# Performance work log

Measured on AMD Instinct MI355X. Metric: run time of the kernel, lower is better.

## Reference

```python
import jax, jax.numpy as jnp
import numpy as np

N = 262144  # nodes
E = 262144  # edges (child -> parent)
X = 128     # x_size
H = 128     # h_size


def setup_inputs() -> dict:
    key = jax.random.key(0)
    ks = jax.random.split(key, 10)
    s = 1.0 / np.sqrt(H)
    return {
        "token_embeds": jax.random.normal(ks[0], (N, X), jnp.float32),
        "h": jax.random.normal(ks[1], (N, H), jnp.float32),
        "c": jax.random.normal(ks[2], (N, H), jnp.float32),
        "src": jax.random.randint(ks[3], (E,), 0, N),
        "dst": jax.random.randint(ks[4], (E,), 0, N),
        "W_iou": jax.random.normal(ks[5], (3 * H, X), jnp.float32) * s,
        "U_iou": jax.random.normal(ks[6], (3 * H, H), jnp.float32) * s,
        "b_iou": jnp.zeros((1, 3 * H), jnp.float32),
        "U_f_w": jax.random.normal(ks[7], (H, H), jnp.float32) * s,
        "U_f_b": jnp.zeros((H,), jnp.float32),
        "W_f_w": jax.random.normal(ks[8], (H, X), jnp.float32) * s,
        "b_f": jnp.zeros((1, H), jnp.float32),
    }


def reference(token_embeds, h, c, src, dst, W_iou, U_iou, b_iou, U_f_w, U_f_b, W_f_w, b_f):
    # message + reduce: gather children's h/c and sum into parent mailboxes
    h_sum = jax.ops.segment_sum(h[src], dst, num_segments=N)  # [N,H]
    c_sum = jax.ops.segment_sum(c[src], dst, num_segments=N)  # [N,H]
    # forget gate is per-node, so sum_k f*c_k == f * sum_k c_k
    f = jax.nn.sigmoid(token_embeds @ W_f_w.T + h @ U_f_w.T + U_f_b + b_f)  # [N,H]
    c_red = f * c_sum
    iou = token_embeds @ W_iou.T + h_sum @ U_iou.T + b_iou  # [N,3H]
    i, o, u = jnp.split(iou, 3, axis=1)
    c_new = jax.nn.sigmoid(i) * jnp.tanh(u) + c_red
    h_new = jax.nn.sigmoid(o) * jnp.tanh(c_new)
    return h_new, c_new
```

## Files before the change

kernel.cpp:

```cpp
#include <hip/hip_runtime.h>
#include <hip/hip_bf16.h>
#include <cstdint>

#define HH 128
#define XX 128

typedef __attribute__((ext_vector_type(8))) short short8;
typedef __attribute__((ext_vector_type(4))) short short4_;
typedef __attribute__((ext_vector_type(4))) float float4_;
typedef __attribute__((ext_vector_type(8))) _Float16 half8_;

__device__ __forceinline__ float sigmoidf_(float x) {
  return 1.f / (1.f + __expf(-x));
}
__device__ __forceinline__ float tanhf_(float x) {
  float e = __expf(-2.f * fabsf(x));
  float t = (1.f - e) / (1.f + e);
  return copysignf(t, x);
}

__global__ __launch_bounds__(256) void hist_kernel(const int* __restrict__ dst,
                                                   int* __restrict__ cnt, int E) {
  int e = blockIdx.x * 256 + threadIdx.x;
  if (e < E) atomicAdd(&cnt[dst[e]], 1);
}

__global__ __launch_bounds__(256) void scan_block_sum(const int* __restrict__ cnt,
                                                      int* __restrict__ bsum) {
  __shared__ int red[256];
  int b = blockIdx.x, t = threadIdx.x;
  int base = b * 1024 + t * 4;
  int s = cnt[base] + cnt[base + 1] + cnt[base + 2] + cnt[base + 3];
  red[t] = s;
  __syncthreads();
  for (int off = 128; off > 0; off >>= 1) {
    if (t < off) red[t] += red[t + off];
    __syncthreads();
  }
  if (t == 0) bsum[b] = red[0];
}

__global__ __launch_bounds__(256) void scan_top(const int* __restrict__ bsum,
                                                int* __restrict__ boff,
                                                int* __restrict__ row_ptr, int N,
                                                int E) {
  __shared__ int tmp[256];
  int t = threadIdx.x;
  int own = bsum[t];
  tmp[t] = own;
  __syncthreads();
  for (int off = 1; off < 256; off <<= 1) {
    int x = (t >= off) ? tmp[t - off] : 0;
    __syncthreads();
    tmp[t] += x;
    __syncthreads();
  }
  boff[t] = tmp[t] - own;
  if (t == 0) row_ptr[N] = E;
}

__global__ __launch_bounds__(256) void scan_fill(const int* __restrict__ cnt,
                                                 const int* __restrict__ boff,
                                                 int* __restrict__ row_ptr,
                                                 int* __restrict__ row_fill) {
  __shared__ int tsum[256];
  int b = blockIdx.x, t = threadIdx.x;
  int base = b * 1024 + t * 4;
  int v0 = cnt[base], v1 = cnt[base + 1], v2 = cnt[base + 2], v3 = cnt[base + 3];
  int s = v0 + v1 + v2 + v3;
  tsum[t] = s;
  __syncthreads();
  for (int off = 1; off < 256; off <<= 1) {
    int x = (t >= off) ? tsum[t - off] : 0;
    __syncthreads();
    tsum[t] += x;
    __syncthreads();
  }
  int excl = tsum[t] - s + boff[b];
  int p0 = excl, p1 = p0 + v0, p2 = p1 + v1, p3 = p2 + v2;
  row_ptr[base] = p0;
  row_ptr[base + 1] = p1;
  row_ptr[base + 2] = p2;
  row_ptr[base + 3] = p3;
  row_fill[base] = p0;
  row_fill[base + 1] = p1;
  row_fill[base + 2] = p2;
  row_fill[base + 3] = p3;
}

__global__ __launch_bounds__(256) void fill_kernel(const int* __restrict__ src,
                                                   const int* __restrict__ dst,
                                                   int* __restrict__ row_fill,
                                                   int* __restrict__ edge_src,
                                                   int E) {
  int e = blockIdx.x * 256 + threadIdx.x;
  if (e >= E) return;
  int pos = atomicAdd(&row_fill[dst[e]], 1);
  edge_src[pos] = src[e];
}

__global__ __launch_bounds__(256) void prep_kernel(
    const float* __restrict__ W_iou, const float* __restrict__ U_iou,
    const float* __restrict__ b_iou, const float* __restrict__ U_f_w,
    const float* __restrict__ U_f_b, const float* __restrict__ W_f_w,
    const float* __restrict__ b_f, unsigned short* __restrict__ Bh,
    float* __restrict__ bias) {
  int tid = blockIdx.x * 256 + threadIdx.x;
  int kg = tid & 3;
  int c16 = (tid >> 2) & 15;
  int ks = (tid >> 6) & 7;
  int w = (tid >> 9) & 7;
  int g = (tid >> 12) & 3;
  int col = w * 16 + c16;
  int kbase = ks * 32 + kg * 8;
#pragma unroll
  for (int j = 0; j < 8; ++j) {
    int k = kbase + j;
    float v;
    if (g < 3) {
      v = (k < 128) ? W_iou[(size_t)(g * 128 + col) * 128 + k]
                    : U_iou[(size_t)(g * 128 + col) * 128 + (k - 128)];
    } else {
      v = (k < 128) ? W_f_w[(size_t)col * 128 + k]
                    : U_f_w[(size_t)col * 128 + (k - 128)];
    }
    Bh[(size_t)tid * 8 + j] = __builtin_bit_cast(unsigned short, (_Float16)v);
  }
  if (tid < 512) {
    int gg = tid >> 7, cc = tid & 127;
    bias[tid] = (gg < 3) ? b_iou[gg * 128 + cc] : (U_f_b[cc] + b_f[cc]);
  }
}


__device__ __forceinline__ void stage_f16(unsigned short* su, int a, int node,
                                          int k4, float4_ v) {
  unsigned short hq[4];
#pragma unroll
  for (int j = 0; j < 4; ++j)
    hq[j] = __builtin_bit_cast(unsigned short, (_Float16)v[j]);
  int off = k4 ^ ((node & 7) << 3);
  *reinterpret_cast<short4_*>(&su[a * 8192 + node * 128 + off]) =
      *reinterpret_cast<const short4_*>(hq);
}

__device__ __forceinline__ half8_ read_frag(const unsigned short* su, int a,
                                            int node, int kbase, int lane) {
  int k = kbase + ((lane >> 4) << 3);
  int off = k ^ ((node & 7) << 3);
  short8 s = *reinterpret_cast<const short8*>(&su[a * 8192 + node * 128 + off]);
  return __builtin_bit_cast(half8_, s);
}

__device__ __forceinline__ int cw(int row, int col) {
  return row * 128 + (col ^ ((row & 7) << 2));
}

__global__ __launch_bounds__(512, 4) void fused_mfma_kernel(
    const float* __restrict__ te, const float* __restrict__ h,
    const float* __restrict__ c, const int* __restrict__ row_ptr,
    const int* __restrict__ edge_src, const unsigned short* __restrict__ Bh,
    const float* __restrict__ bias, float* __restrict__ out_h,
    float* __restrict__ out_c) {
  __shared__ float4_ smem4[5120];
  unsigned short* su = (unsigned short*)smem4;
  float* cf = (float*)smem4 + 12288;

  const int t = threadIdx.x;
  const int node0 = blockIdx.x * 64;

  const int nl = t >> 3;
  const int sub = t & 7;
  const int e0 = row_ptr[node0 + nl];
  const int e1 = row_ptr[node0 + nl + 1];
  int s0 = (e0 < e1) ? edge_src[e0] : 0;
  float4_ ph[4], pc[4];
  if (e0 < e1) {
    const float* hp = h + (size_t)s0 * HH + sub * 16;
    const float* cp = c + (size_t)s0 * HH + sub * 16;
#pragma unroll
    for (int i = 0; i < 4; ++i) {
      ph[i] = *reinterpret_cast<const float4_*>(hp + i * 4);
      pc[i] = *reinterpret_cast<const float4_*>(cp + i * 4);
    }
  }

#pragma unroll
  for (int i = 0; i < 4; ++i) {
    int q = t + i * 512;
    int node = q >> 5;
    int k4 = (q & 31) * 4;
    float4_ v =
        *reinterpret_cast<const float4_*>(te + (size_t)(node0 + node) * XX + k4);
    stage_f16(su, 0, node, k4, v);
    v = *reinterpret_cast<const float4_*>(h + (size_t)(node0 + node) * HH + k4);
    stage_f16(su, 2, node, k4, v);
  }

  {
    float hs[16], cs[16];
#pragma unroll
    for (int j = 0; j < 16; ++j) {
      hs[j] = 0.f;
      cs[j] = 0.f;
    }
    if (e0 < e1) {
#pragma unroll
      for (int i = 0; i < 4; ++i)
#pragma unroll
        for (int j = 0; j < 4; ++j) {
          hs[i * 4 + j] += ph[i][j];
          cs[i * 4 + j] += pc[i][j];
        }
    }
    for (int e = e0 + 1; e < e1; ++e) {
      int s = edge_src[e];
      const float* hp = h + (size_t)s * HH + sub * 16;
      const float* cp = c + (size_t)s * HH + sub * 16;
#pragma unroll
      for (int i = 0; i < 4; ++i) {
        float4_ hv = *reinterpret_cast<const float4_*>(hp + i * 4);
        float4_ cv = *reinterpret_cast<const float4_*>(cp + i * 4);
#pragma unroll
        for (int j = 0; j < 4; ++j) {
          hs[i * 4 + j] += hv[j];
          cs[i * 4 + j] += cv[j];
        }
      }
    }
#pragma unroll
    for (int i = 0; i < 4; ++i) {
      float4_ v = {hs[i * 4], hs[i * 4 + 1], hs[i * 4 + 2], hs[i * 4 + 3]};
      stage_f16(su, 1, nl, sub * 16 + i * 4, v);
      *reinterpret_cast<float4_*>(&cf[cw(nl, sub * 16 + i * 4)]) =
          (float4_){cs[i * 4], cs[i * 4 + 1], cs[i * 4 + 2], cs[i * 4 + 3]};
    }
  }
  __syncthreads();

  const int lane = t & 63;
  const int wave = t >> 6;
  const int wc = wave * 16;
  const int cl = lane & 15;
  const int kq = lane >> 4;

  float4_ acc[4][4];
#pragma unroll
  for (int g = 0; g < 4; ++g) {
    float b = bias[g * 128 + wc + cl];
#pragma unroll
    for (int m = 0; m < 4; ++m) acc[g][m] = (float4_){b, b, b, b};
  }

  for (int ks = 0; ks < 8; ++ks) {
    half8_ bh[4];
#pragma unroll
    for (int g = 0; g < 4; ++g) {
      size_t boff = (size_t)(((g * 8 + wave) * 8 + ks) * 512) + cl * 32 + kq * 8;
      bh[g] = __builtin_bit_cast(half8_,
                                 *reinterpret_cast<const short8*>(&Bh[boff]));
    }
    if (ks < 4) {
      int kbase = ks * 32;
#pragma unroll
      for (int m = 0; m < 4; ++m) {
        half8_ ah = read_frag(su, 0, m * 16 + cl, kbase, lane);
#pragma unroll
        for (int g = 0; g < 4; ++g)
          acc[g][m] =
              __builtin_amdgcn_mfma_f32_16x16x32_f16(ah, bh[g], acc[g][m], 0, 0, 0);
      }
    } else {
      int kbase = (ks - 4) * 32;
#pragma unroll
      for (int m = 0; m < 4; ++m) {
        half8_ ah = read_frag(su, 1, m * 16 + cl, kbase, lane);
        half8_ fh = read_frag(su, 2, m * 16 + cl, kbase, lane);
#pragma unroll
        for (int g = 0; g < 3; ++g)
          acc[g][m] =
              __builtin_amdgcn_mfma_f32_16x16x32_f16(ah, bh[g], acc[g][m], 0, 0, 0);
        acc[3][m] =
            __builtin_amdgcn_mfma_f32_16x16x32_f16(fh, bh[3], acc[3][m], 0, 0, 0);
      }
    }
  }

  float csv[4][4];
#pragma unroll
  for (int m = 0; m < 4; ++m)
#pragma unroll
    for (int r = 0; r < 4; ++r)
      csv[m][r] = cf[cw(m * 16 + kq * 4 + r, wc + cl)];

  __syncthreads();

  float* oh = (float*)smem4;
  float* oc = (float*)smem4 + 8192;

#pragma unroll
  for (int m = 0; m < 4; ++m) {
#pragma unroll
    for (int r = 0; r < 4; ++r) {
      int rowl = m * 16 + kq * 4 + r;
      float ig = sigmoidf_(acc[0][m][r]);
      float og = sigmoidf_(acc[1][m][r]);
      float ug = tanhf_(acc[2][m][r]);
      float fg = sigmoidf_(acc[3][m][r]);
      float cn = fmaf(ig, ug, fg * csv[m][r]);
      int wadr = cw(rowl, wc + cl);
      oc[wadr] = cn;
      oh[wadr] = og * tanhf_(cn);
    }
  }
  __syncthreads();

#pragma unroll
  for (int i = 0; i < 4; ++i) {
    int q = t + i * 512;
    int rr = q >> 5;
    int k4 = (q & 31) * 4;
    int wadr = rr * 128 + (k4 ^ ((rr & 7) << 2));
    *reinterpret_cast<float4_*>(out_h + (size_t)(node0 + rr) * HH + k4) =
        *reinterpret_cast<const float4_*>(&oh[wadr]);
    *reinterpret_cast<float4_*>(out_c + (size_t)(node0 + rr) * HH + k4) =
        *reinterpret_cast<const float4_*>(&oc[wadr]);
  }
}

extern "C" void kernel_launch(void* const* d_in, const int* in_sizes, int n_in,
                              void* d_out, int out_size, void* d_ws, size_t ws_size,
                              hipStream_t stream) {
  const float* te = (const float*)d_in[0];
  const float* h = (const float*)d_in[1];
  const float* c = (const float*)d_in[2];
  const int* src = (const int*)d_in[3];
  const int* dst = (const int*)d_in[4];
  const float* W_iou = (const float*)d_in[5];
  const float* U_iou = (const float*)d_in[6];
  const float* b_iou = (const float*)d_in[7];
  const float* U_f_w = (const float*)d_in[8];
  const float* U_f_b = (const float*)d_in[9];
  const float* W_f_w = (const float*)d_in[10];
  const float* b_f = (const float*)d_in[11];

  const int N = in_sizes[1] / HH;
  const int E = in_sizes[3];

  float* out_h = (float*)d_out;
  float* out_c = out_h + (size_t)N * HH;

  char* ws = (char*)d_ws;
  unsigned short* Bh = (unsigned short*)ws;
  float* bias = (float*)(Bh + 4 * 8 * 8 * 16 * 4 * 8);
  int* cnt = (int*)(bias + 512);
  int* row_ptr = cnt + N;
  int* row_fill = row_ptr + N + 4;
  int* edge_src = row_fill + N;
  int* bsum = edge_src + E;
  int* boff = bsum + 256;

  hipMemsetAsync(cnt, 0, (size_t)N * sizeof(int), stream);

  hist_kernel<<<(E + 255) / 256, 256, 0, stream>>>(dst, cnt, E);
  scan_block_sum<<<N / 1024, 256, 0, stream>>>(cnt, bsum);
  scan_top<<<1, 256, 0, stream>>>(bsum, boff, row_ptr, N, E);
  scan_fill<<<N / 1024, 256, 0, stream>>>(cnt, boff, row_ptr, row_fill);
  fill_kernel<<<(E + 255) / 256, 256, 0, stream>>>(src, dst, row_fill, edge_src, E);

  prep_kernel<<<64, 256, 0, stream>>>(W_iou, U_iou, b_iou, U_f_w, U_f_b, W_f_w,
                                      b_f, Bh, bias);

  fused_mfma_kernel<<<N / 64, 512, 0, stream>>>(te, h, c, row_ptr, edge_src, Bh,
                                                bias, out_h, out_c);
}
```

Baseline: 289.5 us.

## Switch LDS staging to padded rows, pack c_sum as fp16, use pkrtz conversion

Replaces the XOR-swizzled LDS layout with row padding (stride 136) for the fp16 operand tiles and the output staging. The summed child cell state is now stored in LDS as fp16 instead of fp32, which shrinks shared memory from 80KB to about 68KB per block and may allow more blocks per CU. Float-to-half conversion uses the packed round-toward-zero instruction, and bias is added after the MFMA loop instead of seeding the accumulators. Storing c_sum in fp16 and using round-toward-zero reduce precision of the cell-state path.

After: 294.8 us. Within noise of the previous version (+1.8%).

```diff
diff --git a/kernel.cpp b/kernel.cpp
--- a/kernel.cpp
+++ b/kernel.cpp
@@ -4,11 +4,13 @@
 
 #define HH 128
 #define XX 128
+#define RS 136
 
 typedef __attribute__((ext_vector_type(8))) short short8;
-typedef __attribute__((ext_vector_type(4))) short short4_;
 typedef __attribute__((ext_vector_type(4))) float float4_;
 typedef __attribute__((ext_vector_type(8))) _Float16 half8_;
+typedef __attribute__((ext_vector_type(2))) unsigned int uint2_;
+typedef __attribute__((ext_vector_type(4))) unsigned int uint4_;
 
 __device__ __forceinline__ float sigmoidf_(float x) {
   return 1.f / (1.f + __expf(-x));
@@ -133,27 +135,28 @@
 }
 
 
-__device__ __forceinline__ void stage_f16(unsigned short* su, int a, int node,
-                                          int k4, float4_ v) {
-  unsigned short hq[4];
-#pragma unroll
-  for (int j = 0; j < 4; ++j)
-    hq[j] = __builtin_bit_cast(unsigned short, (_Float16)v[j]);
-  int off = k4 ^ ((node & 7) << 3);
-  *reinterpret_cast<short4_*>(&su[a * 8192 + node * 128 + off]) =
-      *reinterpret_cast<const short4_*>(hq);
-}
-
-__device__ __forceinline__ half8_ read_frag(const unsigned short* su, int a,
-                                            int node, int kbase, int lane) {
-  int k = kbase + ((lane >> 4) << 3);
-  int off = k ^ ((node & 7) << 3);
-  short8 s = *reinterpret_cast<const short8*>(&su[a * 8192 + node * 128 + off]);
+__device__ __forceinline__ uint4_ pack8(const float* v) {
+  uint4_ r;
+#pragma unroll
+  for (int i = 0; i < 4; ++i)
+    r[i] = __builtin_bit_cast(unsigned int,
+                              __builtin_amdgcn_cvt_pkrtz(v[2 * i], v[2 * i + 1]));
+  return r;
+}
+
+__device__ __forceinline__ void stage4(unsigned short* su, int baseH, int node,
+                                       int k4, float4_ v) {
+  uint2_ u;
+  u[0] = __builtin_bit_cast(unsigned int, __builtin_amdgcn_cvt_pkrtz(v[0], v[1]));
+  u[1] = __builtin_bit_cast(unsigned int, __builtin_amdgcn_cvt_pkrtz(v[2], v[3]));
+  *reinterpret_cast<uint2_*>(&su[baseH + node * RS + k4]) = u;
+}
+
+__device__ __forceinline__ half8_ read_frag(const unsigned short* su, int baseH,
+                                            int node, int kbase, int kq) {
+  short8 s =
+      *reinterpret_cast<const short8*>(&su[baseH + node * RS + kbase + kq * 8]);
   return __builtin_bit_cast(half8_, s);
-}
-
-__device__ __forceinline__ int cw(int row, int col) {
-  return row * 128 + (col ^ ((row & 7) << 2));
 }
 
 __global__ __launch_bounds__(512, 4) void fused_mfma_kernel(
@@ -162,9 +165,8 @@
     const int* __restrict__ edge_src, const unsigned short* __restrict__ Bh,
     const float* __restrict__ bias, float* __restrict__ out_h,
     float* __restrict__ out_c) {
-  __shared__ float4_ smem4[5120];
+  __shared__ float4_ smem4[4352];
   unsigned short* su = (unsigned short*)smem4;
-  float* cf = (float*)smem4 + 12288;
 
   const int t = threadIdx.x;
   const int node0 = blockIdx.x * 64;
@@ -192,9 +194,9 @@
     int k4 = (q & 31) * 4;
     float4_ v =
         *reinterpret_cast<const float4_*>(te + (size_t)(node0 + node) * XX + k4);
-    stage_f16(su, 0, node, k4, v);
+    stage4(su, 0, node, k4, v);
     v = *reinterpret_cast<const float4_*>(h + (size_t)(node0 + node) * HH + k4);
-    stage_f16(su, 2, node, k4, v);
+    stage4(su, 17408, node, k4, v);
   }
 
   {
@@ -229,11 +231,10 @@
       }
     }
 #pragma unroll
-    for (int i = 0; i < 4; ++i) {
-      float4_ v = {hs[i * 4], hs[i * 4 + 1], hs[i * 4 + 2], hs[i * 4 + 3]};
-      stage_f16(su, 1, nl, sub * 16 + i * 4, v);
-      *reinterpret_cast<float4_*>(&cf[cw(nl, sub * 16 + i * 4)]) =
-          (float4_){cs[i * 4], cs[i * 4 + 1], cs[i * 4 + 2], cs[i * 4 + 3]};
+    for (int i = 0; i < 2; ++i) {
+      int off = nl * RS + sub * 16 + i * 8;
+      *reinterpret_cast<uint4_*>(&su[8704 + off]) = pack8(hs + i * 8);
+      *reinterpret_cast<uint4_*>(&su[26112 + off]) = pack8(cs + i * 8);
     }
   }
   __syncthreads();
@@ -243,14 +244,13 @@
   const int wc = wave * 16;
   const int cl = lane & 15;
   const int kq = lane >> 4;
+  const int col = wc + cl;
 
   float4_ acc[4][4];
 #pragma unroll
-  for (int g = 0; g < 4; ++g) {
-    float b = bias[g * 128 + wc + cl];
-#pragma unroll
-    for (int m = 0; m < 4; ++m) acc[g][m] = (float4_){b, b, b, b};
-  }
+  for (int g = 0; g < 4; ++g)
+#pragma unroll
+    for (int m = 0; m < 4; ++m) acc[g][m] = (float4_){0.f, 0.f, 0.f, 0.f};
 
   for (int ks = 0; ks < 8; ++ks) {
     half8_ bh[4];
@@ -264,55 +264,60 @@
       int kbase = ks * 32;
 #pragma unroll
       for (int m = 0; m < 4; ++m) {
-        half8_ ah = read_frag(su, 0, m * 16 + cl, kbase, lane);
+        half8_ ah = read_frag(su, 0, m * 16 + cl, kbase, kq);
 #pragma unroll
         for (int g = 0; g < 4; ++g)
-          acc[g][m] =
-              __builtin_amdgcn_mfma_f32_16x16x32_f16(ah, bh[g], acc[g][m], 0, 0, 0);
+          acc[g][m] = __builtin_amdgcn_mfma_f32_16x16x32_f16(ah, bh[g],
+                                                             acc[g][m], 0, 0, 0);
       }
     } else {
       int kbase = (ks - 4) * 32;
 #pragma unroll
       for (int m = 0; m < 4; ++m) {
-        half8_ ah = read_frag(su, 1, m * 16 + cl, kbase, lane);
-        half8_ fh = read_frag(su, 2, m * 16 + cl, kbase, lane);
+        half8_ ah = read_frag(su, 8704, m * 16 + cl, kbase, kq);
+        half8_ fh = read_frag(su, 17408, m * 16 + cl, kbase, kq);
 #pragma unroll
         for (int g = 0; g < 3; ++g)
-          acc[g][m] =
-              __builtin_amdgcn_mfma_f32_16x16x32_f16(ah, bh[g], acc[g][m], 0, 0, 0);
-        acc[3][m] =
-            __builtin_amdgcn_mfma_f32_16x16x32_f16(fh, bh[3], acc[3][m], 0, 0, 0);
+          acc[g][m] = __builtin_amdgcn_mfma_f32_16x16x32_f16(ah, bh[g],
+                                                             acc[g][m], 0, 0, 0);
+        acc[3][m] = __builtin_amdgcn_mfma_f32_16x16x32_f16(fh, bh[3],
+                                                           acc[3][m], 0, 0, 0);
       }
     }
   }
 
+  const float bi = bias[col];
+  const float bo = bias[128 + col];
+  const float bu = bias[256 + col];
+  const float bf = bias[384 + col];
   float csv[4][4];
 #pragma unroll
   for (int m = 0; m < 4; ++m)
 #pragma unroll
-    for (int r = 0; r < 4; ++r)
-      csv[m][r] = cf[cw(m * 16 + kq * 4 + r, wc + cl)];
-
+    for (int r = 0; r < 4; ++r) {
+      int row = m * 16 + kq * 4 + r;
+      unsigned short hb = su[26112 + row * RS + col];
+      csv[m][r] = (float)__builtin_bit_cast(_Float16, hb);
+    }
   __syncthreads();
 
   float* oh = (float*)smem4;
-  float* oc = (float*)smem4 + 8192;
-
-#pragma unroll
-  for (int m = 0; m < 4; ++m) {
+  float* oc = (float*)smem4 + 8704;
+
+#pragma unroll
+  for (int m = 0; m < 4; ++m)
 #pragma unroll
     for (int r = 0; r < 4; ++r) {
       int rowl = m * 16 + kq * 4 + r;
-      float ig = sigmoidf_(acc[0][m][r]);
-      float og = sigmoidf_(acc[1][m][r]);
-      float ug = tanhf_(acc[2][m][r]);
-      float fg = sigmoidf_(acc[3][m][r]);
+      float ig = sigmoidf_(acc[0][m][r] + bi);
+      float og = sigmoidf_(acc[1][m][r] + bo);
+      float ug = tanhf_(acc[2][m][r] + bu);
+      float fg = sigmoidf_(acc[3][m][r] + bf);
       float cn = fmaf(ig, ug, fg * csv[m][r]);
-      int wadr = cw(rowl, wc + cl);
+      int wadr = rowl * RS + col;
       oc[wadr] = cn;
       oh[wadr] = og * tanhf_(cn);
     }
-  }
   __syncthreads();
 
 #pragma unroll
@@ -320,7 +325,7 @@
     int q = t + i * 512;
     int rr = q >> 5;
     int k4 = (q & 31) * 4;
-    int wadr = rr * 128 + (k4 ^ ((rr & 7) << 2));
+    int wadr = rr * RS + k4;
     *reinterpret_cast<float4_*>(out_h + (size_t)(node0 + rr) * HH + k4) =
         *reinterpret_cast<const float4_*>(&oh[wadr]);
     *reinterpret_cast<float4_*>(out_c + (size_t)(node0 + rr) * HH + k4) =
```
